# Optimization experiments

Hardware: AMD Instinct MI355X
Metric: run time of the kernel (lower is better)

## Reference

```python
import jax, jax.numpy as jnp
import numpy as np

NUM_HEADS = 8
KEY_DIM = 16
D_HEAD = 64  # attn_ratio(4) * key_dim


def setup_inputs() -> dict:
    key = jax.random.key(0)
    ks = jax.random.split(key, 13)
    f = jnp.float32
    x = jax.random.normal(ks[0], (2, 256, 56, 56), dtype=f)
    wq = jax.random.normal(ks[1], (128, 256), dtype=f) * 0.05
    sq = jax.random.uniform(ks[2], (128,), dtype=f)
    bq = jax.random.normal(ks[3], (128,), dtype=f) * 0.05
    wk = jax.random.normal(ks[4], (128, 256), dtype=f) * 0.05
    sk = jax.random.uniform(ks[5], (128,), dtype=f)
    bk = jax.random.normal(ks[6], (128,), dtype=f) * 0.05
    wv = jax.random.normal(ks[7], (512, 256), dtype=f) * 0.05
    sv = jax.random.uniform(ks[8], (512,), dtype=f)
    bv = jax.random.normal(ks[9], (512,), dtype=f) * 0.05
    wp = jax.random.normal(ks[10], (256, 512), dtype=f) * 0.05
    sp = jax.random.uniform(ks[11], (256,), dtype=f)
    bp = jax.random.normal(ks[12], (256,), dtype=f) * 0.05
    return dict(x=x, wq=wq, sq=sq, bq=bq, wk=wk, sk=sk, bk=bk,
                wv=wv, sv=sv, bv=bv, wp=wp, sp=sp, bp=bp)


def _conv1x1_bn(x, w, s, b):
    # 1x1 conv (no bias) + folded BatchNorm (eval): per-channel affine
    y = jnp.einsum('oc,bchw->bohw', w, x)
    return y * s[None, :, None, None] + b[None, :, None, None]


def reference(x, wq, sq, bq, wk, sk, bk, wv, sv, bv, wp, sp, bp):
    b, c, h, w = x.shape
    n = h * w
    q = _conv1x1_bn(x, wq, sq, bq).reshape(b, NUM_HEADS, KEY_DIM, n)
    k = _conv1x1_bn(x, wk, sk, bk).reshape(b, NUM_HEADS, KEY_DIM, n)
    v = _conv1x1_bn(x, wv, sv, bv).reshape(b, NUM_HEADS, D_HEAD, n)
    # scores: q^T k, NO 1/sqrt(key_dim) scaling (faithful to source)
    attn = jax.nn.softmax(jnp.einsum('bhdn,bhdm->bhnm', q, k), axis=-1)
    # out = attn @ v^T -> (b,h,n,d), then back to (b, dh, H, W)
    o = jnp.einsum('bhnm,bhdm->bhdn', attn, v).reshape(b, NUM_HEADS * D_HEAD, h, w)
    return _conv1x1_bn(o, wp, sp, bp)
```

## Files before the change

kernel.cpp:

```cpp
#include <hip/hip_runtime.h>


typedef short  s16x8 __attribute__((ext_vector_type(8)));
typedef float  f32x4 __attribute__((ext_vector_type(4)));
typedef int    i32x4 __attribute__((ext_vector_type(4)));
typedef unsigned short u16;
typedef unsigned short u16x4 __attribute__((ext_vector_type(4)));

__device__ __forceinline__ u16 f2bf(float f) {
    unsigned u = __builtin_bit_cast(unsigned, f);
    u += 0x7FFF + ((u >> 16) & 1);
    return (u16)(u >> 16);
}
__device__ __forceinline__ f32x4 mfma32(s16x8 a, s16x8 b, f32x4 c) {
    return __builtin_amdgcn_mfma_f32_16x16x32_bf16(a, b, c, 0, 0, 0);
}
__device__ __forceinline__ int cvtpk(float lo, float hi) {
    int r;
    asm("v_cvt_pk_bf16_f32 %0, %1, %2" : "=v"(r) : "v"(lo), "v"(hi));
    return r;
}

__global__ __launch_bounds__(256) void xtw_kernel(
    const float* __restrict__ x, u16* __restrict__ xpk,
    const float* __restrict__ wq, const float* __restrict__ sq,
    const float* __restrict__ wk, const float* __restrict__ sk,
    const float* __restrict__ wv, const float* __restrict__ sv,
    const float* __restrict__ wp, const float* __restrict__ sp,
    u16* __restrict__ wqpk, u16* __restrict__ wkpk,
    u16* __restrict__ wvpk, u16* __restrict__ wppk)
{
    const int t = threadIdx.x;
    if (blockIdx.z == 2) {
        if (blockIdx.y >= 4) return;
        int ch = (blockIdx.y * 49 + blockIdx.x) * 256 + t;
        const float *W, *S; u16* dst; int nkc;
        if (ch < 4096)        { W = wq; S = sq; dst = wqpk; nkc = 8; }
        else if (ch < 8192)   { W = wk; S = sk; dst = wkpk; nkc = 8;  ch -= 4096; }
        else if (ch < 24576)  { W = wv; S = sv; dst = wvpk; nkc = 8;  ch -= 8192; }
        else if (ch < 40960)  { W = wp; S = sp; dst = wppk; nkc = 16; ch -= 24576; }
        else return;
        const int lane = ch & 63, kc = (ch >> 6) % nkc, rt = (ch >> 6) / nkc;
        const int l15 = lane & 15, q = lane >> 4;
        const int row = rt * 16 + l15, C = nkc * 32;
        const float sc = S[row];
        const float* src = &W[row * C + kc * 32 + q * 8];
        s16x8 o;
        #pragma unroll
        for (int j = 0; j < 8; j++) o[j] = (short)f2bf(src[j] * sc);
        *(s16x8*)&dst[ch * 8] = o;
        return;
    }
    const int b = blockIdx.z, c0 = blockIdx.y * 32, n0 = blockIdx.x * 64;
    __shared__ float lds[32][65];
    const int nl = t & 63, cl = t >> 6;
    #pragma unroll
    for (int i = 0; i < 8; i++) {
        const int c = cl + i * 4;
        lds[c][nl] = x[(b * 256 + c0 + c) * 3136 + n0 + nl];
    }
    __syncthreads();
    {
        const int t16l = t >> 6, lane = t & 63;
        const int l15 = lane & 15, q = lane >> 4;
        s16x8 o;
        #pragma unroll
        for (int j = 0; j < 8; j++)
            o[j] = (short)f2bf(lds[q * 8 + j][t16l * 16 + l15]);
        const int tg = (n0 >> 4) + t16l, kg = blockIdx.y;
        *(s16x8*)&xpk[(((b * 196 + tg) * 8 + kg) * 64 + lane) * 8] = o;
    }
}

__global__ __launch_bounds__(256, 4) void qkv_kernel(
    const u16* __restrict__ xpk,
    const u16* __restrict__ wqpk, const u16* __restrict__ wkpk, const u16* __restrict__ wvpk,
    const float* __restrict__ bq, const float* __restrict__ bk, const float* __restrict__ bv,
    u16* __restrict__ qws, u16* __restrict__ kws, u16* __restrict__ vpk)
{
    const int b = blockIdx.z, rt = blockIdx.y;
    const int t = threadIdx.x, wave = t >> 6, lane = t & 63;
    const int l15 = lane & 15, quad = lane >> 4;
    const f32x4 z = {0.f, 0.f, 0.f, 0.f};

    if (rt < 2) {
        const float qs = 1.44269504088896f;
        const int wl = wave & 1, fh = wave >> 1;
        const int m_t = blockIdx.x * 2 + wl;
        const int m0  = m_t * 16;
        s16x8 a8[8];
        #pragma unroll
        for (int kc8 = 0; kc8 < 8; kc8++)
            a8[kc8] = *(const s16x8*)&xpk[(((b * 196 + m_t) * 8 + kc8) * 64 + lane) * 8];
        f32x4 aq_[2] = {z, z}, ak_[2] = {z, z};
        #pragma unroll
        for (int kc8 = 0; kc8 < 8; kc8++) {
            #pragma unroll
            for (int ff = 0; ff < 2; ff++) {
                const int f = fh * 2 + ff;
                const int wi = (((rt * 4 + f) * 8 + kc8) * 64 + lane) * 8;
                s16x8 bfq = *(const s16x8*)&wqpk[wi];
                aq_[ff] = mfma32(a8[kc8], bfq, aq_[ff]);
                s16x8 bfk = *(const s16x8*)&wkpk[wi];
                ak_[ff] = mfma32(a8[kc8], bfk, ak_[ff]);
            }
        }
        #pragma unroll
        for (int ff = 0; ff < 2; ff++) {
            const int f   = fh * 2 + ff;
            const int och = rt * 64 + f * 16 + l15;
            const float biq = bq[och], bik = bk[och];
            const int h = och >> 4;
            #pragma unroll
            for (int r = 0; r < 4; r++) {
                const int tok = m0 + quad * 4 + r;
                qws[((b * 8 + h) * 3136 + tok) * 16 + l15] = f2bf((aq_[ff][r] + biq) * qs);
                kws[((b * 8 + h) * 3136 + tok) * 16 + l15] = f2bf(ak_[ff][r] + bik);
            }
        }
    } else {
        const int h0 = (rt - 2) * 2, h1 = h0 + 1;
        const int c = blockIdx.x >> 1, half = blockIdx.x & 1;
        s16x8 a80[8], a81[8];
        #pragma unroll
        for (int kc8 = 0; kc8 < 8; kc8++) {
            a80[kc8] = *(const s16x8*)&wvpk[(((h0 * 4 + wave) * 8 + kc8) * 64 + lane) * 8];
            a81[kc8] = *(const s16x8*)&wvpk[(((h1 * 4 + wave) * 8 + kc8) * 64 + lane) * 8];
        }
        f32x4 ac0[2] = {z, z}, ac1[2] = {z, z};
        #pragma unroll
        for (int kc8 = 0; kc8 < 8; kc8++) {
            #pragma unroll
            for (int ff = 0; ff < 2; ff++) {
                const int f = half * 2 + ff;
                s16x8 bf = *(const s16x8*)&xpk[(((b * 196 + c * 4 + f) * 8 + kc8) * 64 + lane) * 8];
                ac0[ff] = mfma32(a80[kc8], bf, ac0[ff]);
                ac1[ff] = mfma32(a81[kc8], bf, ac1[ff]);
            }
        }
        #pragma unroll
        for (int hh = 0; hh < 2; hh++) {
            const int h = hh ? h1 : h0;
            const f32x4* ac = hh ? ac1 : ac0;
            const int och0v = h * 64 + wave * 16;
            u16* vdst = &vpk[(((b * 8 + h) * 49 + c) * 8) * 512];
            #pragma unroll
            for (int r = 0; r < 4; r++) {
                const float bi = bv[och0v + quad * 4 + r];
                const int lane_r8 = ((l15 >> 2) * 16 + quad * 4 + r) * 8;
                #pragma unroll
                for (int ff = 0; ff < 2; ff++) {
                    const int idx = (half * 4 + wave) * 512 + lane_r8 + ff * 4 + (l15 & 3);
                    vdst[idx] = f2bf(ac[ff][r] + bi);
                }
            }
        }
    }
}

__global__ __launch_bounds__(64) void attn_kernel(
    const u16* __restrict__ qws, const u16* __restrict__ kws,
    const u16* __restrict__ vpk, u16* __restrict__ opk)
{
    const int bh   = blockIdx.x;
    const int nb   = blockIdx.y * 32;
    const int lane = threadIdx.x;
    const int l15  = lane & 15, quad = lane >> 4;

    s16x8 aq[2];
    #pragma unroll
    for (int u = 0; u < 2; u++) {
        aq[u] = (s16x8){0, 0, 0, 0, 0, 0, 0, 0};
        if (quad < 2)
            aq[u] = *(const s16x8*)&qws[(bh * 3136 + nb + u * 16 + l15) * 16 + quad * 8];
    }
    s16x8 ones;
    #pragma unroll
    for (int i = 0; i < 8; i++) ones[i] = (short)0x3F80;

    const u16* krow = &kws[(bh * 3136 + l15) * 16 + (quad & 1) * 8];
    const u16* vb   = &vpk[bh * 49 * 4096 + lane * 8];

    f32x4 acc[2][4], acc5[2];
    #pragma unroll
    for (int u = 0; u < 2; u++) {
        #pragma unroll
        for (int dt = 0; dt < 4; dt++) acc[u][dt] = (f32x4){0.f, 0.f, 0.f, 0.f};
        acc5[u] = (f32x4){0.f, 0.f, 0.f, 0.f};
    }
    const f32x4 z = {0.f, 0.f, 0.f, 0.f};

    s16x8 kfA[4], vfA[8], kfB[4], vfB[8];
    auto loadK = [&](s16x8* kf, int c) {
        #pragma unroll
        for (int ii = 0; ii < 4; ii++)
            kf[ii] = *(const s16x8*)&krow[(c * 64 + ii * 16) * 16];
    };
    auto loadV = [&](s16x8* vf, int c) {
        #pragma unroll
        for (int i = 0; i < 8; i++)
            vf[i] = *(const s16x8*)&vb[(c * 8 + i) * 512];
    };
    auto compute = [&](const s16x8* kf, const s16x8* vf) {
        #pragma unroll
        for (int u = 0; u < 2; u++) {
            f32x4 s[4];
            #pragma unroll
            for (int ii = 0; ii < 4; ii++) s[ii] = mfma32(kf[ii], aq[u], z);
            float e[4][4];
            #pragma unroll
            for (int ii = 0; ii < 4; ii++)
                #pragma unroll
                for (int r = 0; r < 4; r++)
                    e[ii][r] = __builtin_amdgcn_exp2f(s[ii][r]);
            s16x8 pf[2];
            #pragma unroll
            for (int c32 = 0; c32 < 2; c32++) {
                i32x4 pk;
                pk[0] = cvtpk(e[2 * c32][0],     e[2 * c32][1]);
                pk[1] = cvtpk(e[2 * c32][2],     e[2 * c32][3]);
                pk[2] = cvtpk(e[2 * c32 + 1][0], e[2 * c32 + 1][1]);
                pk[3] = cvtpk(e[2 * c32 + 1][2], e[2 * c32 + 1][3]);
                pf[c32] = __builtin_bit_cast(s16x8, pk);
            }
            __builtin_amdgcn_s_setprio(1);
            #pragma unroll
            for (int c32 = 0; c32 < 2; c32++) {
                #pragma unroll
                for (int dt = 0; dt < 4; dt++)
                    acc[u][dt] = mfma32(vf[c32 * 4 + dt], pf[c32], acc[u][dt]);
                acc5[u] = mfma32(ones, pf[c32], acc5[u]);
            }
            __builtin_amdgcn_s_setprio(0);
        }
    };

    loadK(kfA, 0); loadV(vfA, 0);
    #pragma unroll 1
    for (int c = 0; c < 49; c += 2) {
        if (c + 1 < 49) { loadK(kfB, c + 1); loadV(vfB, c + 1); }
        compute(kfA, vfA);
        if (c + 2 < 49) { loadK(kfA, c + 2); loadV(vfA, c + 2); }
        if (c + 1 < 49) compute(kfB, vfB);
    }

    const int bq_ = bh >> 3, h = bh & 7;
    #pragma unroll
    for (int u = 0; u < 2; u++) {
        const float inv = 1.0f / acc5[u][0];
        const int tt = blockIdx.y * 2 + u;
        u16* ob = &opk[((bq_ * 196 + tt) * 16) * 512];
        #pragma unroll
        for (int dt = 0; dt < 4; dt++) {
            u16x4 o4;
            #pragma unroll
            for (int r = 0; r < 4; r++) o4[r] = f2bf(acc[u][dt][r] * inv);
            *(u16x4*)&ob[(h * 2 + (dt >> 1)) * 512 +
                         (((dt & 1) * 2 + (quad >> 1)) * 16 + l15) * 8 +
                         (quad & 1) * 4] = o4;
        }
    }
}

__global__ __launch_bounds__(256, 4) void proj_kernel(
    const u16* __restrict__ opk, const u16* __restrict__ wppk,
    const float* __restrict__ bp, float* __restrict__ out)
{
    const int b = blockIdx.z, n0 = blockIdx.x * 16;
    const int och0 = blockIdx.y * 64 + (threadIdx.x >> 6) * 16;
    const int lane = threadIdx.x & 63;
    const int l15 = lane & 15, quad = lane >> 4;
    const f32x4 z = {0.f, 0.f, 0.f, 0.f};

    const int och_t = blockIdx.y * 4 + (threadIdx.x >> 6);
    s16x8 a8[16];
    #pragma unroll
    for (int kc = 0; kc < 16; kc++)
        a8[kc] = *(const s16x8*)&wppk[((och_t * 16 + kc) * 64 + lane) * 8];
    f32x4 acc = z;
    #pragma unroll
    for (int kc = 0; kc < 16; kc++) {
        s16x8 bf = *(const s16x8*)&opk[(((b * 196 + blockIdx.x) * 16 + kc) * 64 + lane) * 8];
        acc = mfma32(a8[kc], bf, acc);
    }
    #pragma unroll
    for (int r = 0; r < 4; r++) {
        const int och = och0 + quad * 4 + r;
        out[(b * 256 + och) * 3136 + n0 + l15] = acc[r] + bp[och];
    }
}

extern "C" void kernel_launch(void* const* d_in, const int* in_sizes, int n_in,
                              void* d_out, int out_size, void* d_ws, size_t ws_size,
                              hipStream_t stream) {
    const float* x  = (const float*)d_in[0];
    const float* wq = (const float*)d_in[1];
    const float* sq = (const float*)d_in[2];
    const float* bq = (const float*)d_in[3];
    const float* wk = (const float*)d_in[4];
    const float* sk = (const float*)d_in[5];
    const float* bk = (const float*)d_in[6];
    const float* wv = (const float*)d_in[7];
    const float* sv = (const float*)d_in[8];
    const float* bv = (const float*)d_in[9];
    const float* wp = (const float*)d_in[10];
    const float* sp = (const float*)d_in[11];
    const float* bp = (const float*)d_in[12];
    float* out = (float*)d_out;

    u16* qws  = (u16*)d_ws;
    u16* kws  = qws + 802816;
    u16* vpk  = kws + 802816;
    u16* R    = vpk + 3211264;
    u16* xpk  = R;
    u16* opk  = R;
    u16* wqpk = R + 3211264;
    u16* wkpk = wqpk + 32768;
    u16* wvpk = wkpk + 32768;
    u16* wppk = wvpk + 131072;

    xtw_kernel<<<dim3(49, 8, 3), 256, 0, stream>>>(x, xpk, wq, sq, wk, sk,
                                                   wv, sv, wp, sp,
                                                   wqpk, wkpk, wvpk, wppk);
    qkv_kernel<<<dim3(98, 6, 2), 256, 0, stream>>>(xpk, wqpk, wkpk, wvpk,
                                                   bq, bk, bv, qws, kws, vpk);
    attn_kernel<<<dim3(16, 98), 64, 0, stream>>>(qws, kws, vpk, opk);
    proj_kernel<<<dim3(196, 4, 2), 256, 0, stream>>>(opk, wppk, bp, out);
}
```

Baseline: 151.8 us.

## Fuse pack, QKV and attention into a persistent kernel with grid barriers

Merges the x/weight packing, the QKV projection and the attention kernels into one persistent kernel of 512 blocks. Each stage uses a grid-stride loop over its old work items, and stages are separated by global atomic-counter barriers. Stores that later stages read become agent-scope atomic stores. The aim is to remove two kernel launches and the gaps between them, at the cost of barrier spin time and a fixed 4-wave block shape for attention, where some waves sit idle. The barrier counter lives inside the opk scratch region; this only works because it is reset every call and overwritten only after the last barrier.

```diff
diff --git a/kernel.cpp b/kernel.cpp
--- a/kernel.cpp
+++ b/kernel.cpp
@@ -6,6 +6,9 @@
 typedef int    i32x4 __attribute__((ext_vector_type(4)));
 typedef unsigned short u16;
 typedef unsigned short u16x4 __attribute__((ext_vector_type(4)));
+typedef unsigned long long u64;
+
+#define NB 512
 
 __device__ __forceinline__ u16 f2bf(float f) {
     unsigned u = __builtin_bit_cast(unsigned, f);
@@ -20,244 +23,277 @@
     asm("v_cvt_pk_bf16_f32 %0, %1, %2" : "=v"(r) : "v"(lo), "v"(hi));
     return r;
 }
-
-__global__ __launch_bounds__(256) void xtw_kernel(
-    const float* __restrict__ x, u16* __restrict__ xpk,
+__device__ __forceinline__ void st16_wt(u16* p, s16x8 v) {
+    u64 q0 = *(const u64*)&v;
+    u64 q1 = ((const u64*)&v)[1];
+    __hip_atomic_store((u64*)p,     q0, __ATOMIC_RELAXED, __HIP_MEMORY_SCOPE_AGENT);
+    __hip_atomic_store((u64*)p + 1, q1, __ATOMIC_RELAXED, __HIP_MEMORY_SCOPE_AGENT);
+}
+__device__ __forceinline__ void st2_wt(u16* p, u16 v) {
+    __hip_atomic_store(p, v, __ATOMIC_RELAXED, __HIP_MEMORY_SCOPE_AGENT);
+}
+__device__ __forceinline__ void gbar(unsigned* ctr, unsigned target) {
+    __syncthreads();
+    __threadfence();
+    if (threadIdx.x == 0) {
+        __hip_atomic_fetch_add(ctr, 1u, __ATOMIC_ACQ_REL, __HIP_MEMORY_SCOPE_AGENT);
+        while (__hip_atomic_load(ctr, __ATOMIC_ACQUIRE, __HIP_MEMORY_SCOPE_AGENT) < target)
+            __builtin_amdgcn_s_sleep(2);
+    }
+    __syncthreads();
+}
+
+__global__ __launch_bounds__(256, 2) void fused_kernel(
+    const float* __restrict__ x,
     const float* __restrict__ wq, const float* __restrict__ sq,
     const float* __restrict__ wk, const float* __restrict__ sk,
     const float* __restrict__ wv, const float* __restrict__ sv,
     const float* __restrict__ wp, const float* __restrict__ sp,
+    const float* __restrict__ bq, const float* __restrict__ bk,
+    const float* __restrict__ bv,
+    unsigned* __restrict__ ctr,
+    u16* __restrict__ qws, u16* __restrict__ kws, u16* __restrict__ vpk,
+    u16* __restrict__ xpk, u16* __restrict__ opk,
     u16* __restrict__ wqpk, u16* __restrict__ wkpk,
     u16* __restrict__ wvpk, u16* __restrict__ wppk)
 {
-    const int t = threadIdx.x;
-    if (blockIdx.z == 2) {
-        if (blockIdx.y >= 4) return;
-        int ch = (blockIdx.y * 49 + blockIdx.x) * 256 + t;
-        const float *W, *S; u16* dst; int nkc;
-        if (ch < 4096)        { W = wq; S = sq; dst = wqpk; nkc = 8; }
-        else if (ch < 8192)   { W = wk; S = sk; dst = wkpk; nkc = 8;  ch -= 4096; }
-        else if (ch < 24576)  { W = wv; S = sv; dst = wvpk; nkc = 8;  ch -= 8192; }
-        else if (ch < 40960)  { W = wp; S = sp; dst = wppk; nkc = 16; ch -= 24576; }
-        else return;
-        const int lane = ch & 63, kc = (ch >> 6) % nkc, rt = (ch >> 6) / nkc;
-        const int l15 = lane & 15, q = lane >> 4;
-        const int row = rt * 16 + l15, C = nkc * 32;
-        const float sc = S[row];
-        const float* src = &W[row * C + kc * 32 + q * 8];
-        s16x8 o;
-        #pragma unroll
-        for (int j = 0; j < 8; j++) o[j] = (short)f2bf(src[j] * sc);
-        *(s16x8*)&dst[ch * 8] = o;
-        return;
-    }
-    const int b = blockIdx.z, c0 = blockIdx.y * 32, n0 = blockIdx.x * 64;
+    const int blk = blockIdx.x;
+    const int t   = threadIdx.x;
     __shared__ float lds[32][65];
-    const int nl = t & 63, cl = t >> 6;
-    #pragma unroll
-    for (int i = 0; i < 8; i++) {
-        const int c = cl + i * 4;
-        lds[c][nl] = x[(b * 256 + c0 + c) * 3136 + n0 + nl];
-    }
-    __syncthreads();
+
+    for (int it = blk; it < 980; it += NB) {
+        if (it < 196) {
+            int ch = it * 256 + t;
+            const float *W, *S; u16* dst; int nkc; bool ok = true;
+            if (ch < 4096)        { W = wq; S = sq; dst = wqpk; nkc = 8; }
+            else if (ch < 8192)   { W = wk; S = sk; dst = wkpk; nkc = 8;  ch -= 4096; }
+            else if (ch < 24576)  { W = wv; S = sv; dst = wvpk; nkc = 8;  ch -= 8192; }
+            else if (ch < 40960)  { W = wp; S = sp; dst = wppk; nkc = 16; ch -= 24576; }
+            else ok = false;
+            if (ok) {
+                const int lane = ch & 63, kc = (ch >> 6) % nkc, rt = (ch >> 6) / nkc;
+                const int l15 = lane & 15, q = lane >> 4;
+                const int row = rt * 16 + l15, C = nkc * 32;
+                const float sc = S[row];
+                const float* src = &W[row * C + kc * 32 + q * 8];
+                s16x8 o;
+                #pragma unroll
+                for (int j = 0; j < 8; j++) o[j] = (short)f2bf(src[j] * sc);
+                st16_wt(&dst[ch * 8], o);
+            }
+        } else {
+            const int j  = it - 196;
+            const int b  = j / 392, r = j % 392;
+            const int kg = r / 49, c0 = kg * 32, n0 = (r % 49) * 64;
+            const int nl = t & 63, cl = t >> 6;
+            #pragma unroll
+            for (int i = 0; i < 8; i++) {
+                const int c = cl + i * 4;
+                lds[c][nl] = x[(b * 256 + c0 + c) * 3136 + n0 + nl];
+            }
+            __syncthreads();
+            {
+                const int t16l = t >> 6, lane = t & 63;
+                const int l15 = lane & 15, q = lane >> 4;
+                s16x8 o;
+                #pragma unroll
+                for (int jj = 0; jj < 8; jj++)
+                    o[jj] = (short)f2bf(lds[q * 8 + jj][t16l * 16 + l15]);
+                const int tg = (n0 >> 4) + t16l;
+                st16_wt(&xpk[(((b * 196 + tg) * 8 + kg) * 64 + lane) * 8], o);
+            }
+            __syncthreads();
+        }
+    }
+    gbar(ctr, NB);
+
+    for (int it = blk; it < 1176; it += NB) {
+        const int bx = it % 98, rt = (it / 98) % 6, b = it / 588;
+        const int wave = t >> 6, lane = t & 63;
+        const int l15 = lane & 15, quad = lane >> 4;
+        const f32x4 z = {0.f, 0.f, 0.f, 0.f};
+
+        if (rt < 2) {
+            const float qs = 1.44269504088896f;
+            const int wl = wave & 1, fh = wave >> 1;
+            const int m_t = bx * 2 + wl;
+            const int m0  = m_t * 16;
+            s16x8 a8[8];
+            #pragma unroll
+            for (int kc8 = 0; kc8 < 8; kc8++)
+                a8[kc8] = *(const s16x8*)&xpk[(((b * 196 + m_t) * 8 + kc8) * 64 + lane) * 8];
+            f32x4 aq_[2] = {z, z}, ak_[2] = {z, z};
+            #pragma unroll
+            for (int kc8 = 0; kc8 < 8; kc8++) {
+                #pragma unroll
+                for (int ff = 0; ff < 2; ff++) {
+                    const int f = fh * 2 + ff;
+                    const int wi = (((rt * 4 + f) * 8 + kc8) * 64 + lane) * 8;
+                    s16x8 bfq = *(const s16x8*)&wqpk[wi];
+                    aq_[ff] = mfma32(a8[kc8], bfq, aq_[ff]);
+                    s16x8 bfk = *(const s16x8*)&wkpk[wi];
+                    ak_[ff] = mfma32(a8[kc8], bfk, ak_[ff]);
+                }
+            }
+            #pragma unroll
+            for (int ff = 0; ff < 2; ff++) {
+                const int f   = fh * 2 + ff;
+                const int och = rt * 64 + f * 16 + l15;
+                const float biq = bq[och], bik = bk[och];
+                const int h = och >> 4;
+                #pragma unroll
+                for (int r = 0; r < 4; r++) {
+                    const int tok = m0 + quad * 4 + r;
+                    st2_wt(&qws[((b * 8 + h) * 3136 + tok) * 16 + l15],
+                           f2bf((aq_[ff][r] + biq) * qs));
+                    st2_wt(&kws[((b * 8 + h) * 3136 + tok) * 16 + l15],
+                           f2bf(ak_[ff][r] + bik));
+                }
+            }
+        } else {
+            const int h0 = (rt - 2) * 2, h1 = h0 + 1;
+            const int c = bx >> 1, half = bx & 1;
+            s16x8 a80[8], a81[8];
+            #pragma unroll
+            for (int kc8 = 0; kc8 < 8; kc8++) {
+                a80[kc8] = *(const s16x8*)&wvpk[(((h0 * 4 + wave) * 8 + kc8) * 64 + lane) * 8];
+                a81[kc8] = *(const s16x8*)&wvpk[(((h1 * 4 + wave) * 8 + kc8) * 64 + lane) * 8];
+            }
+            f32x4 ac0[2] = {z, z}, ac1[2] = {z, z};
+            #pragma unroll
+            for (int kc8 = 0; kc8 < 8; kc8++) {
+                #pragma unroll
+                for (int ff = 0; ff < 2; ff++) {
+                    const int f = half * 2 + ff;
+                    s16x8 bf = *(const s16x8*)&xpk[(((b * 196 + c * 4 + f) * 8 + kc8) * 64 + lane) * 8];
+                    ac0[ff] = mfma32(a80[kc8], bf, ac0[ff]);
+                    ac1[ff] = mfma32(a81[kc8], bf, ac1[ff]);
+                }
+            }
+            #pragma unroll
+            for (int hh = 0; hh < 2; hh++) {
+                const int h = hh ? h1 : h0;
+                const f32x4* ac = hh ? ac1 : ac0;
+                const int och0v = h * 64 + wave * 16;
+                u16* vdst = &vpk[(((b * 8 + h) * 49 + c) * 8) * 512];
+                #pragma unroll
+                for (int r = 0; r < 4; r++) {
+                    const float bi = bv[och0v + quad * 4 + r];
+                    const int lane_r8 = ((l15 >> 2) * 16 + quad * 4 + r) * 8;
+                    #pragma unroll
+                    for (int ff = 0; ff < 2; ff++) {
+                        const int idx = (half * 4 + wave) * 512 + lane_r8 + ff * 4 + (l15 & 3);
+                        st2_wt(&vdst[idx], f2bf(ac[ff][r] + bi));
+                    }
+                }
+            }
+        }
+    }
+    gbar(ctr, 2 * NB);
+
     {
-        const int t16l = t >> 6, lane = t & 63;
-        const int l15 = lane & 15, q = lane >> 4;
-        s16x8 o;
-        #pragma unroll
-        for (int j = 0; j < 8; j++)
-            o[j] = (short)f2bf(lds[q * 8 + j][t16l * 16 + l15]);
-        const int tg = (n0 >> 4) + t16l, kg = blockIdx.y;
-        *(s16x8*)&xpk[(((b * 196 + tg) * 8 + kg) * 64 + lane) * 8] = o;
-    }
-}
-
-__global__ __launch_bounds__(256, 4) void qkv_kernel(
-    const u16* __restrict__ xpk,
-    const u16* __restrict__ wqpk, const u16* __restrict__ wkpk, const u16* __restrict__ wvpk,
-    const float* __restrict__ bq, const float* __restrict__ bk, const float* __restrict__ bv,
-    u16* __restrict__ qws, u16* __restrict__ kws, u16* __restrict__ vpk)
-{
-    const int b = blockIdx.z, rt = blockIdx.y;
-    const int t = threadIdx.x, wave = t >> 6, lane = t & 63;
-    const int l15 = lane & 15, quad = lane >> 4;
-    const f32x4 z = {0.f, 0.f, 0.f, 0.f};
-
-    if (rt < 2) {
-        const float qs = 1.44269504088896f;
-        const int wl = wave & 1, fh = wave >> 1;
-        const int m_t = blockIdx.x * 2 + wl;
-        const int m0  = m_t * 16;
-        s16x8 a8[8];
-        #pragma unroll
-        for (int kc8 = 0; kc8 < 8; kc8++)
-            a8[kc8] = *(const s16x8*)&xpk[(((b * 196 + m_t) * 8 + kc8) * 64 + lane) * 8];
-        f32x4 aq_[2] = {z, z}, ak_[2] = {z, z};
-        #pragma unroll
-        for (int kc8 = 0; kc8 < 8; kc8++) {
-            #pragma unroll
-            for (int ff = 0; ff < 2; ff++) {
-                const int f = fh * 2 + ff;
-                const int wi = (((rt * 4 + f) * 8 + kc8) * 64 + lane) * 8;
-                s16x8 bfq = *(const s16x8*)&wqpk[wi];
-                aq_[ff] = mfma32(a8[kc8], bfq, aq_[ff]);
-                s16x8 bfk = *(const s16x8*)&wkpk[wi];
-                ak_[ff] = mfma32(a8[kc8], bfk, ak_[ff]);
-            }
-        }
-        #pragma unroll
-        for (int ff = 0; ff < 2; ff++) {
-            const int f   = fh * 2 + ff;
-            const int och = rt * 64 + f * 16 + l15;
-            const float biq = bq[och], bik = bk[och];
-            const int h = och >> 4;
-            #pragma unroll
-            for (int r = 0; r < 4; r++) {
-                const int tok = m0 + quad * 4 + r;
-                qws[((b * 8 + h) * 3136 + tok) * 16 + l15] = f2bf((aq_[ff][r] + biq) * qs);
-                kws[((b * 8 + h) * 3136 + tok) * 16 + l15] = f2bf(ak_[ff][r] + bik);
-            }
-        }
-    } else {
-        const int h0 = (rt - 2) * 2, h1 = h0 + 1;
-        const int c = blockIdx.x >> 1, half = blockIdx.x & 1;
-        s16x8 a80[8], a81[8];
-        #pragma unroll
-        for (int kc8 = 0; kc8 < 8; kc8++) {
-            a80[kc8] = *(const s16x8*)&wvpk[(((h0 * 4 + wave) * 8 + kc8) * 64 + lane) * 8];
-            a81[kc8] = *(const s16x8*)&wvpk[(((h1 * 4 + wave) * 8 + kc8) * 64 + lane) * 8];
-        }
-        f32x4 ac0[2] = {z, z}, ac1[2] = {z, z};
-        #pragma unroll
-        for (int kc8 = 0; kc8 < 8; kc8++) {
-            #pragma unroll
-            for (int ff = 0; ff < 2; ff++) {
-                const int f = half * 2 + ff;
-                s16x8 bf = *(const s16x8*)&xpk[(((b * 196 + c * 4 + f) * 8 + kc8) * 64 + lane) * 8];
-                ac0[ff] = mfma32(a80[kc8], bf, ac0[ff]);
-                ac1[ff] = mfma32(a81[kc8], bf, ac1[ff]);
-            }
-        }
-        #pragma unroll
-        for (int hh = 0; hh < 2; hh++) {
-            const int h = hh ? h1 : h0;
-            const f32x4* ac = hh ? ac1 : ac0;
-            const int och0v = h * 64 + wave * 16;
-            u16* vdst = &vpk[(((b * 8 + h) * 49 + c) * 8) * 512];
-            #pragma unroll
-            for (int r = 0; r < 4; r++) {
-                const float bi = bv[och0v + quad * 4 + r];
-                const int lane_r8 = ((l15 >> 2) * 16 + quad * 4 + r) * 8;
-                #pragma unroll
-                for (int ff = 0; ff < 2; ff++) {
-                    const int idx = (half * 4 + wave) * 512 + lane_r8 + ff * 4 + (l15 & 3);
-                    vdst[idx] = f2bf(ac[ff][r] + bi);
-                }
-            }
-        }
-    }
-}
-
-__global__ __launch_bounds__(64) void attn_kernel(
-    const u16* __restrict__ qws, const u16* __restrict__ kws,
-    const u16* __restrict__ vpk, u16* __restrict__ opk)
-{
-    const int bh   = blockIdx.x;
-    const int nb   = blockIdx.y * 32;
-    const int lane = threadIdx.x;
-    const int l15  = lane & 15, quad = lane >> 4;
-
-    s16x8 aq[2];
-    #pragma unroll
-    for (int u = 0; u < 2; u++) {
-        aq[u] = (s16x8){0, 0, 0, 0, 0, 0, 0, 0};
-        if (quad < 2)
-            aq[u] = *(const s16x8*)&qws[(bh * 3136 + nb + u * 16 + l15) * 16 + quad * 8];
-    }
-    s16x8 ones;
-    #pragma unroll
-    for (int i = 0; i < 8; i++) ones[i] = (short)0x3F80;
-
-    const u16* krow = &kws[(bh * 3136 + l15) * 16 + (quad & 1) * 8];
-    const u16* vb   = &vpk[bh * 49 * 4096 + lane * 8];
-
-    f32x4 acc[2][4], acc5[2];
-    #pragma unroll
-    for (int u = 0; u < 2; u++) {
-        #pragma unroll
-        for (int dt = 0; dt < 4; dt++) acc[u][dt] = (f32x4){0.f, 0.f, 0.f, 0.f};
-        acc5[u] = (f32x4){0.f, 0.f, 0.f, 0.f};
-    }
-    const f32x4 z = {0.f, 0.f, 0.f, 0.f};
-
-    s16x8 kfA[4], vfA[8], kfB[4], vfB[8];
-    auto loadK = [&](s16x8* kf, int c) {
-        #pragma unroll
-        for (int ii = 0; ii < 4; ii++)
-            kf[ii] = *(const s16x8*)&krow[(c * 64 + ii * 16) * 16];
-    };
-    auto loadV = [&](s16x8* vf, int c) {
-        #pragma unroll
-        for (int i = 0; i < 8; i++)
-            vf[i] = *(const s16x8*)&vb[(c * 8 + i) * 512];
-    };
-    auto compute = [&](const s16x8* kf, const s16x8* vf) {
-        #pragma unroll
-        for (int u = 0; u < 2; u++) {
-            f32x4 s[4];
-            #pragma unroll
-            for (int ii = 0; ii < 4; ii++) s[ii] = mfma32(kf[ii], aq[u], z);
-            float e[4][4];
-            #pragma unroll
-            for (int ii = 0; ii < 4; ii++)
-                #pragma unroll
-                for (int r = 0; r < 4; r++)
-                    e[ii][r] = __builtin_amdgcn_exp2f(s[ii][r]);
-            s16x8 pf[2];
-            #pragma unroll
-            for (int c32 = 0; c32 < 2; c32++) {
-                i32x4 pk;
-                pk[0] = cvtpk(e[2 * c32][0],     e[2 * c32][1]);
-                pk[1] = cvtpk(e[2 * c32][2],     e[2 * c32][3]);
-                pk[2] = cvtpk(e[2 * c32 + 1][0], e[2 * c32 + 1][1]);
-                pk[3] = cvtpk(e[2 * c32 + 1][2], e[2 * c32 + 1][3]);
-                pf[c32] = __builtin_bit_cast(s16x8, pk);
-            }
-            __builtin_amdgcn_s_setprio(1);
-            #pragma unroll
-            for (int c32 = 0; c32 < 2; c32++) {
-                #pragma unroll
-                for (int dt = 0; dt < 4; dt++)
-                    acc[u][dt] = mfma32(vf[c32 * 4 + dt], pf[c32], acc[u][dt]);
-                acc5[u] = mfma32(ones, pf[c32], acc5[u]);
-            }
-            __builtin_amdgcn_s_setprio(0);
-        }
-    };
-
-    loadK(kfA, 0); loadV(vfA, 0);
-    #pragma unroll 1
-    for (int c = 0; c < 49; c += 2) {
-        if (c + 1 < 49) { loadK(kfB, c + 1); loadV(vfB, c + 1); }
-        compute(kfA, vfA);
-        if (c + 2 < 49) { loadK(kfA, c + 2); loadV(vfA, c + 2); }
-        if (c + 1 < 49) compute(kfB, vfB);
-    }
-
-    const int bq_ = bh >> 3, h = bh & 7;
-    #pragma unroll
-    for (int u = 0; u < 2; u++) {
-        const float inv = 1.0f / acc5[u][0];
-        const int tt = blockIdx.y * 2 + u;
-        u16* ob = &opk[((bq_ * 196 + tt) * 16) * 512];
-        #pragma unroll
-        for (int dt = 0; dt < 4; dt++) {
-            u16x4 o4;
-            #pragma unroll
-            for (int r = 0; r < 4; r++) o4[r] = f2bf(acc[u][dt][r] * inv);
-            *(u16x4*)&ob[(h * 2 + (dt >> 1)) * 512 +
-                         (((dt & 1) * 2 + (quad >> 1)) * 16 + l15) * 8 +
-                         (quad & 1) * 4] = o4;
+        const int wave = t >> 6, lane = t & 63;
+        const int cls = blk & 7;
+        const int il  = (blk >> 3) * 4 + wave;
+        if (il < 196) {
+            const int bh = cls + 8 * (il & 1);
+            const int yq = il >> 1;
+            const int nb = yq * 32;
+            const int l15 = lane & 15, quad = lane >> 4;
+
+            s16x8 aq[2];
+            #pragma unroll
+            for (int u = 0; u < 2; u++) {
+                aq[u] = (s16x8){0, 0, 0, 0, 0, 0, 0, 0};
+                if (quad < 2)
+                    aq[u] = *(const s16x8*)&qws[(bh * 3136 + nb + u * 16 + l15) * 16 + quad * 8];
+            }
+            s16x8 ones;
+            #pragma unroll
+            for (int i = 0; i < 8; i++) ones[i] = (short)0x3F80;
+
+            const u16* krow = &kws[(bh * 3136 + l15) * 16 + (quad & 1) * 8];
+            const u16* vb   = &vpk[bh * 49 * 4096 + lane * 8];
+
+            f32x4 acc[2][4], acc5[2];
+            #pragma unroll
+            for (int u = 0; u < 2; u++) {
+                #pragma unroll
+                for (int dt = 0; dt < 4; dt++) acc[u][dt] = (f32x4){0.f, 0.f, 0.f, 0.f};
+                acc5[u] = (f32x4){0.f, 0.f, 0.f, 0.f};
+            }
+            const f32x4 z = {0.f, 0.f, 0.f, 0.f};
+
+            s16x8 kfA[4], vfA[8], kfB[4], vfB[8];
+            auto loadK = [&](s16x8* kf, int c) {
+                #pragma unroll
+                for (int ii = 0; ii < 4; ii++)
+                    kf[ii] = *(const s16x8*)&krow[(c * 64 + ii * 16) * 16];
+            };
+            auto loadV = [&](s16x8* vf, int c) {
+                #pragma unroll
+                for (int i = 0; i < 8; i++)
+                    vf[i] = *(const s16x8*)&vb[(c * 8 + i) * 512];
+            };
+            auto compute = [&](const s16x8* kf, const s16x8* vf) {
+                #pragma unroll
+                for (int u = 0; u < 2; u++) {
+                    f32x4 s[4];
+                    #pragma unroll
+                    for (int ii = 0; ii < 4; ii++) s[ii] = mfma32(kf[ii], aq[u], z);
+                    float e[4][4];
+                    #pragma unroll
+                    for (int ii = 0; ii < 4; ii++)
+                        #pragma unroll
+                        for (int r = 0; r < 4; r++)
+                            e[ii][r] = __builtin_amdgcn_exp2f(s[ii][r]);
+                    s16x8 pf[2];
+                    #pragma unroll
+                    for (int c32 = 0; c32 < 2; c32++) {
+                        i32x4 pk;
+                        pk[0] = cvtpk(e[2 * c32][0],     e[2 * c32][1]);
+                        pk[1] = cvtpk(e[2 * c32][2],     e[2 * c32][3]);
+                        pk[2] = cvtpk(e[2 * c32 + 1][0], e[2 * c32 + 1][1]);
+                        pk[3] = cvtpk(e[2 * c32 + 1][2], e[2 * c32 + 1][3]);
+                        pf[c32] = __builtin_bit_cast(s16x8, pk);
+                    }
+                    __builtin_amdgcn_s_setprio(1);
+                    #pragma unroll
+                    for (int c32 = 0; c32 < 2; c32++) {
+                        #pragma unroll
+                        for (int dt = 0; dt < 4; dt++)
+                            acc[u][dt] = mfma32(vf[c32 * 4 + dt], pf[c32], acc[u][dt]);
+                        acc5[u] = mfma32(ones, pf[c32], acc5[u]);
+                    }
+                    __builtin_amdgcn_s_setprio(0);
+                }
+            };
+
+            loadK(kfA, 0); loadV(vfA, 0);
+            #pragma unroll 1
+            for (int c = 0; c < 49; c += 2) {
+                if (c + 1 < 49) { loadK(kfB, c + 1); loadV(vfB, c + 1); }
+                compute(kfA, vfA);
+                if (c + 2 < 49) { loadK(kfA, c + 2); loadV(vfA, c + 2); }
+                if (c + 1 < 49) compute(kfB, vfB);
+            }
+
+            const int bq_ = bh >> 3, h = bh & 7;
+            #pragma unroll
+            for (int u = 0; u < 2; u++) {
+                const float inv = 1.0f / acc5[u][0];
+                const int tt = yq * 2 + u;
+                u16* ob = &opk[((bq_ * 196 + tt) * 16) * 512];
+                #pragma unroll
+                for (int dt = 0; dt < 4; dt++) {
+                    u16x4 o4;
+                    #pragma unroll
+                    for (int r = 0; r < 4; r++) o4[r] = f2bf(acc[u][dt][r] * inv);
+                    *(u16x4*)&ob[(h * 2 + (dt >> 1)) * 512 +
+                                 (((dt & 1) * 2 + (quad >> 1)) * 16 + l15) * 8 +
+                                 (quad & 1) * 4] = o4;
+                }
+            }
         }
     }
 }
@@ -319,11 +355,11 @@
     u16* wvpk = wkpk + 32768;
     u16* wppk = wvpk + 131072;
 
-    xtw_kernel<<<dim3(49, 8, 3), 256, 0, stream>>>(x, xpk, wq, sq, wk, sk,
-                                                   wv, sv, wp, sp,
-                                                   wqpk, wkpk, wvpk, wppk);
-    qkv_kernel<<<dim3(98, 6, 2), 256, 0, stream>>>(xpk, wqpk, wkpk, wvpk,
-                                                   bq, bk, bv, qws, kws, vpk);
-    attn_kernel<<<dim3(16, 98), 64, 0, stream>>>(qws, kws, vpk, opk);
+    unsigned* ctr = (unsigned*)(R + 3000000);
+    hipMemsetAsync(ctr, 0, 8, stream);
+
+    fused_kernel<<<dim3(NB), dim3(256), 0, stream>>>(
+        x, wq, sq, wk, sk, wv, sv, wp, sp, bq, bk, bv,
+        ctr, qws, kws, vpk, xpk, opk, wqpk, wkpk, wvpk, wppk);
     proj_kernel<<<dim3(196, 4, 2), 256, 0, stream>>>(opk, wppk, bp, out);
 }
```

Result: slower. 322.2 us (+112.3%).
